# Optimization experiments

Hardware: AMD Instinct MI355X
Metric: run time of the kernel (lower is better)

The kernel has to match this reference:

```python
import jax, jax.numpy as jnp
import numpy as np

LORA_RANK = 16
LORA_ALPHA = 32.0
LORA_SCALE = LORA_ALPHA / LORA_RANK
W_BITS = 8
A_BITS = 8


def fake_quant(x, bits):
    """Symmetric per-tensor fake quantization with straight-through estimator."""
    qmax = 2.0 ** (bits - 1) - 1.0
    scale = jnp.maximum(jnp.max(jnp.abs(x)), 1e-8) / qmax
    q = jnp.clip(jnp.round(x / scale), -qmax, qmax) * scale
    return x + jax.lax.stop_gradient(q - x)  # STE


def quant_linear_lora(x, W, b, A, B):
    # x: [..., in], W: [out, in], A: [r, in], B: [out, r]
    xq = fake_quant(x, A_BITS)
    Wq = fake_quant(W, W_BITS)
    base = jnp.einsum('bsi,oi->bso', xq, Wq) + b
    lora = jnp.einsum('bsr,or->bso', jnp.einsum('bsi,ri->bsr', x, A), B)
    return base + LORA_SCALE * lora


def setup_inputs() -> dict:
    key = jax.random.key(0)
    ks = jax.random.split(key, 9)
    n_embd, d_ff, B_, S = 1024, 4096, 4, 2048
    s_in = 1.0 / np.sqrt(n_embd)
    s_ff = 1.0 / np.sqrt(d_ff)
    return {
        'hidden_states': jax.random.normal(ks[0], (B_, S, n_embd), jnp.float32),
        'W_fc': jax.random.normal(ks[1], (d_ff, n_embd), jnp.float32) * s_in,
        'b_fc': jax.random.normal(ks[2], (d_ff,), jnp.float32) * 0.02,
        'A_fc': jax.random.normal(ks[3], (LORA_RANK, n_embd), jnp.float32) * s_in,
        'B_fc': jax.random.normal(ks[4], (d_ff, LORA_RANK), jnp.float32) * 0.01,
        'W_proj': jax.random.normal(ks[5], (n_embd, d_ff), jnp.float32) * s_ff,
        'b_proj': jax.random.normal(ks[6], (n_embd,), jnp.float32) * 0.02,
        'A_proj': jax.random.normal(ks[7], (LORA_RANK, d_ff), jnp.float32) * s_ff,
        'B_proj': jax.random.normal(ks[8], (n_embd, LORA_RANK), jnp.float32) * 0.01,
    }


def reference(hidden_states, W_fc, b_fc, A_fc, B_fc, W_proj, b_proj, A_proj, B_proj):
    h = quant_linear_lora(hidden_states, W_fc, b_fc, A_fc, B_fc)
    h = jax.nn.gelu(h, approximate=False)  # nn.GELU() default = exact erf GELU
    h = quant_linear_lora(h, W_proj, b_proj, A_proj, B_proj)
    return h
```

## Files before the change

kernel.cpp:

```cpp
#include <hip/hip_runtime.h>
#include <stdint.h>

using i32x4 = __attribute__((ext_vector_type(4))) int;
using f32x4 = __attribute__((ext_vector_type(4))) float;
using f16x4 = __attribute__((ext_vector_type(4))) _Float16;

#define M_TOK 8192
#define N_EMB 1024
#define D_FF  4096

__device__ __forceinline__ void async_lds16(void* lds, const void* g) {
  __builtin_amdgcn_global_load_lds(
      (const __attribute__((address_space(1))) void*)g,
      (__attribute__((address_space(3))) void*)lds, 16, 0, 0);
}

__global__ void zero_slots_k(unsigned* s) {
  if (threadIdx.x < 16) s[threadIdx.x] = 0u;
}

__global__ void absmax_k(const float* __restrict__ p, long n, unsigned* __restrict__ slot) {
  long i = ((long)blockIdx.x * blockDim.x + threadIdx.x) * 4;
  long stride = (long)gridDim.x * blockDim.x * 4;
  float m = 0.f;
  for (; i < n; i += stride) {
    float4 v = *(const float4*)(p + i);
    m = fmaxf(m, fmaxf(fmaxf(fabsf(v.x), fabsf(v.y)), fmaxf(fabsf(v.z), fabsf(v.w))));
  }
  for (int o = 32; o; o >>= 1) m = fmaxf(m, __shfl_xor(m, o));
  __shared__ float sm[4];
  if ((threadIdx.x & 63) == 0) sm[threadIdx.x >> 6] = m;
  __syncthreads();
  if (threadIdx.x == 0) {
    m = fmaxf(fmaxf(sm[0], sm[1]), fmaxf(sm[2], sm[3]));
    atomicMax(slot, __float_as_uint(m));
  }
}

__global__ void quant_k(const float* __restrict__ p, int8_t* __restrict__ q, long n,
                        const unsigned* __restrict__ slot) {
  float inv = 127.f / fmaxf(__uint_as_float(*slot), 1e-8f);
  long i = ((long)blockIdx.x * blockDim.x + threadIdx.x) * 4;
  long stride = (long)gridDim.x * blockDim.x * 4;
  for (; i < n; i += stride) {
    float4 v = *(const float4*)(p + i);
    int b0 = (int)fminf(fmaxf(rintf(v.x * inv), -127.f), 127.f);
    int b1 = (int)fminf(fmaxf(rintf(v.y * inv), -127.f), 127.f);
    int b2 = (int)fminf(fmaxf(rintf(v.z * inv), -127.f), 127.f);
    int b3 = (int)fminf(fmaxf(rintf(v.w * inv), -127.f), 127.f);
    int w = (b0 & 0xff) | ((b1 & 0xff) << 8) | ((b2 & 0xff) << 16) | ((b3 & 0xff) << 24);
    *(int*)(q + i) = w;
  }
}

__global__ void prep_bfrag_k(const float* __restrict__ A, _Float16* __restrict__ Bp, int K) {
  int s = blockIdx.x;
  int l = threadIdx.x;
  int r = l & 15, g = l >> 4;
  float4 v = *(const float4*)(A + (long)r * K + s * 16 + g * 4);
  f16x4 h;
  h[0] = (_Float16)v.x; h[1] = (_Float16)v.y; h[2] = (_Float16)v.z; h[3] = (_Float16)v.w;
  *(f16x4*)(Bp + ((long)s * 64 + l) * 4) = h;
}

__global__ __launch_bounds__(512) void lora_quant_k(
    const float* __restrict__ X, const _Float16* __restrict__ Bpre,
    const unsigned* __restrict__ slot, int8_t* __restrict__ Q,
    float* __restrict__ T, int K) {
  int lane = threadIdx.x & 63, wave = threadIdx.x >> 6;
  int row0 = blockIdx.x * 16;
  int r = lane & 15, g = lane >> 4;
  float inv = 127.f / fmaxf(__uint_as_float(*slot), 1e-8f);

  int kPerWave = K >> 3;
  int kbase = wave * kPerWave;
  const float* xrow = X + (long)(row0 + r) * K;
  int8_t* qrow = Q + (long)(row0 + r) * K;

  f32x4 acc = {0.f, 0.f, 0.f, 0.f};
  int nsteps = kPerWave >> 4;
#pragma unroll 4
  for (int s = 0; s < nsteps; s++) {
    int k = kbase + s * 16 + g * 4;
    float4 v = *(const float4*)(xrow + k);
    int b0 = (int)fminf(fmaxf(rintf(v.x * inv), -127.f), 127.f);
    int b1 = (int)fminf(fmaxf(rintf(v.y * inv), -127.f), 127.f);
    int b2 = (int)fminf(fmaxf(rintf(v.z * inv), -127.f), 127.f);
    int b3 = (int)fminf(fmaxf(rintf(v.w * inv), -127.f), 127.f);
    *(int*)(qrow + k) = (b0 & 0xff) | ((b1 & 0xff) << 8) | ((b2 & 0xff) << 16) | ((b3 & 0xff) << 24);
    f16x4 a;
    a[0] = (_Float16)v.x; a[1] = (_Float16)v.y; a[2] = (_Float16)v.z; a[3] = (_Float16)v.w;
    int gs = (kbase + s * 16) >> 4;
    f16x4 b = *(const f16x4*)(Bpre + ((long)gs * 64 + lane) * 4);
    acc = __builtin_amdgcn_mfma_f32_16x16x16f16(a, b, acc, 0, 0, 0);
  }

  __shared__ float part[8][16][17];
#pragma unroll
  for (int j = 0; j < 4; j++) part[wave][g * 4 + j][r] = acc[j];
  __syncthreads();
  int t = threadIdx.x;
  if (t < 256) {
    int m = t >> 4, rr = t & 15;
    float sum = 0.f;
#pragma unroll
    for (int w = 0; w < 8; w++) sum += part[w][m][rr];
    T[(long)(row0 + m) * 16 + rr] = 2.0f * sum;
  }
}

template <bool GELU>
__global__ __launch_bounds__(256, 3) void gemm_q8(
    const int8_t* __restrict__ Aq, const int8_t* __restrict__ Bq,
    int M, int N, int K,
    const unsigned* __restrict__ sa, const unsigned* __restrict__ sb,
    const float* __restrict__ bias,
    const float* __restrict__ T,
    const float* __restrict__ Bl,
    float* __restrict__ C, unsigned* hmax) {
  __shared__ __align__(16) int8_t As[16384];
  __shared__ __align__(16) int8_t Bs[16384];

  int bn = blockIdx.x * 128;
  int bm = blockIdx.y * 128;

  int t = threadIdx.x;
  int lane = t & 63, wave = t >> 6;
  int wr = wave >> 1, wc = wave & 1;
  int l16 = lane & 15, lq = lane >> 4;

  int ldst[4];
  const int8_t* srcA[4];
  const int8_t* srcB[4];
#pragma unroll
  for (int i = 0; i < 4; i++) {
    int s = i * 256 + t;
    int row = s >> 3;
    int col = s & 7;
    ldst[i] = s * 16;
    srcA[i] = Aq + (long)(bm + row) * K + col * 16;
    srcB[i] = Bq + (long)(bn + row) * K + col * 16;
  }

  int aoff[4], boff[4];
#pragma unroll
  for (int mf = 0; mf < 4; mf++) aoff[mf] = (wr * 64 + mf * 16 + l16) * 128 + lq * 16;
#pragma unroll
  for (int nf = 0; nf < 4; nf++) boff[nf] = (wc * 64 + nf * 16 + l16) * 128 + lq * 16;

  i32x4 acc[4][4] = {};
  int KT = K >> 7;

  for (int kt = 0; kt < KT; ++kt) {
    long ko = (long)kt * 128;
#pragma unroll
    for (int i = 0; i < 4; i++) async_lds16(As + ldst[i], srcA[i] + ko);
#pragma unroll
    for (int i = 0; i < 4; i++) async_lds16(Bs + ldst[i], srcB[i] + ko);
    __syncthreads();

#pragma unroll
    for (int kh = 0; kh < 2; kh++) {
      int kx = kh * 64;
      i32x4 av[4], bv[4];
#pragma unroll
      for (int mf = 0; mf < 4; mf++) av[mf] = *(const i32x4*)(As + aoff[mf] + kx);
#pragma unroll
      for (int nf = 0; nf < 4; nf++) bv[nf] = *(const i32x4*)(Bs + boff[nf] + kx);
#pragma unroll
      for (int mf = 0; mf < 4; mf++)
#pragma unroll
        for (int nf = 0; nf < 4; nf++)
          acc[mf][nf] = __builtin_amdgcn_mfma_i32_16x16x64_i8(av[mf], bv[nf], acc[mf][nf], 0, 0, 0);
    }
    __syncthreads();
  }

  float s = (fmaxf(__uint_as_float(*sa), 1e-8f) * (1.f / 127.f)) *
            (fmaxf(__uint_as_float(*sb), 1e-8f) * (1.f / 127.f));

  f16x4 af[4], bf[4];
#pragma unroll
  for (int mf = 0; mf < 4; mf++) {
    int m = bm + wr * 64 + mf * 16 + l16;
    float4 tv = *(const float4*)(T + (long)m * 16 + lq * 4);
    f16x4 v; v[0] = (_Float16)tv.x; v[1] = (_Float16)tv.y; v[2] = (_Float16)tv.z; v[3] = (_Float16)tv.w;
    af[mf] = v;
  }
#pragma unroll
  for (int nf = 0; nf < 4; nf++) {
    int n = bn + wc * 64 + nf * 16 + l16;
    float4 bv4 = *(const float4*)(Bl + (long)n * 16 + lq * 4);
    f16x4 v; v[0] = (_Float16)bv4.x; v[1] = (_Float16)bv4.y; v[2] = (_Float16)bv4.z; v[3] = (_Float16)bv4.w;
    bf[nf] = v;
  }
  float bias_v[4];
#pragma unroll
  for (int nf = 0; nf < 4; nf++) bias_v[nf] = bias[bn + wc * 64 + nf * 16 + l16];

  float lmax = 0.f;
#pragma unroll
  for (int mf = 0; mf < 4; mf++) {
#pragma unroll
    for (int nf = 0; nf < 4; nf++) {
      f32x4 fa = __builtin_amdgcn_mfma_f32_16x16x16f16(af[mf], bf[nf], f32x4{0.f, 0.f, 0.f, 0.f}, 0, 0, 0);
      int n = bn + wc * 64 + nf * 16 + l16;
#pragma unroll
      for (int j = 0; j < 4; j++) {
        int m = bm + wr * 64 + mf * 16 + lq * 4 + j;
        float v = s * (float)acc[mf][nf][j] + bias_v[nf] + fa[j];
        if constexpr (GELU) {
          v = 0.5f * v * (1.0f + erff(v * 0.70710678118654752f));
          lmax = fmaxf(lmax, fabsf(v));
        }
        C[(long)m * N + n] = v;
      }
    }
  }
  if constexpr (GELU) {
    for (int o = 32; o; o >>= 1) lmax = fmaxf(lmax, __shfl_xor(lmax, o));
    if (lane == 0) atomicMax(hmax, __float_as_uint(lmax));
  }
}

extern "C" void kernel_launch(void* const* d_in, const int* in_sizes, int n_in,
                              void* d_out, int out_size, void* d_ws, size_t ws_size,
                              hipStream_t stream) {
  const float* x   = (const float*)d_in[0];
  const float* Wfc = (const float*)d_in[1];
  const float* bfc = (const float*)d_in[2];
  const float* Afc = (const float*)d_in[3];
  const float* Bfc = (const float*)d_in[4];
  const float* Wpj = (const float*)d_in[5];
  const float* bpj = (const float*)d_in[6];
  const float* Apj = (const float*)d_in[7];
  const float* Bpj = (const float*)d_in[8];
  float* out = (float*)d_out;

  char* ws = (char*)d_ws;
  unsigned* slots = (unsigned*)ws;
  int8_t* qx  = (int8_t*)(ws + 256);
  int8_t* qwf = qx  + (size_t)M_TOK * N_EMB;
  int8_t* qwp = qwf + (size_t)D_FF * N_EMB;
  int8_t* qh  = qwp + (size_t)N_EMB * D_FF;
  float*  t1  = (float*)(qh + (size_t)M_TOK * D_FF);
  float*  t2  = t1  + (size_t)M_TOK * 16;
  _Float16* Bp1 = (_Float16*)(t2 + (size_t)M_TOK * 16);
  _Float16* Bp2 = Bp1 + (size_t)N_EMB * 16;
  float*  h   = (float*)(Bp2 + (size_t)D_FF * 16);

  zero_slots_k<<<1, 64, 0, stream>>>(slots);
  absmax_k<<<1024, 256, 0, stream>>>(x,   (long)M_TOK * N_EMB, slots + 0);
  absmax_k<<<1024, 256, 0, stream>>>(Wfc, (long)D_FF * N_EMB,  slots + 1);
  absmax_k<<<1024, 256, 0, stream>>>(Wpj, (long)N_EMB * D_FF,  slots + 2);

  quant_k<<<2048, 256, 0, stream>>>(Wfc, qwf, (long)D_FF * N_EMB, slots + 1);
  quant_k<<<2048, 256, 0, stream>>>(Wpj, qwp, (long)N_EMB * D_FF, slots + 2);

  prep_bfrag_k<<<N_EMB / 16, 64, 0, stream>>>(Afc, Bp1, N_EMB);
  prep_bfrag_k<<<D_FF / 16, 64, 0, stream>>>(Apj, Bp2, D_FF);

  lora_quant_k<<<M_TOK / 16, 512, 0, stream>>>(x, Bp1, slots + 0, qx, t1, N_EMB);

  gemm_q8<true><<<dim3(D_FF / 128, M_TOK / 128), 256, 0, stream>>>(
      qx, qwf, M_TOK, D_FF, N_EMB, slots + 0, slots + 1, bfc, t1, Bfc, h, slots + 3);

  lora_quant_k<<<M_TOK / 16, 512, 0, stream>>>(h, Bp2, slots + 3, qh, t2, D_FF);

  gemm_q8<false><<<dim3(N_EMB / 128, M_TOK / 128), 256, 0, stream>>>(
      qh, qwp, M_TOK, N_EMB, D_FF, slots + 3, slots + 2, bpj, t2, Bpj, out, nullptr);
}
```

Before: 314.7 us.

## Store quantized operands as exact bf16 and use bf16 MFMA GEMMs

Quantized integer values are now stored as bf16 (exact for values up to 127) instead of int8, and both GEMMs switch from i8 MFMA 16x16x64 to bf16 MFMA 16x16x32 with a 64-wide K tile. This doubles the operand bytes and halves the math rate per instruction relative to int8, presumably to try a different MFMA path or to avoid some int8 issue. The launch-bounds occupancy hint is dropped and workspace buffers are reorganized, with qx aliasing qh.

```diff
diff --git a/kernel.cpp b/kernel.cpp
--- a/kernel.cpp
+++ b/kernel.cpp
@@ -1,9 +1,9 @@
 #include <hip/hip_runtime.h>
 #include <stdint.h>
 
-using i32x4 = __attribute__((ext_vector_type(4))) int;
-using f32x4 = __attribute__((ext_vector_type(4))) float;
-using f16x4 = __attribute__((ext_vector_type(4))) _Float16;
+using f32x4  = __attribute__((ext_vector_type(4))) float;
+using f16x4  = __attribute__((ext_vector_type(4))) _Float16;
+using bf16x8 = __attribute__((ext_vector_type(8))) short;
 
 #define M_TOK 8192
 #define N_EMB 1024
@@ -13,6 +13,10 @@
   __builtin_amdgcn_global_load_lds(
       (const __attribute__((address_space(1))) void*)g,
       (__attribute__((address_space(3))) void*)lds, 16, 0, 0);
+}
+
+__device__ __forceinline__ unsigned short bf16_exact(float f) {
+  return (unsigned short)(__float_as_uint(f) >> 16);
 }
 
 __global__ void zero_slots_k(unsigned* s) {
@@ -37,19 +41,19 @@
   }
 }
 
-__global__ void quant_k(const float* __restrict__ p, int8_t* __restrict__ q, long n,
+__global__ void quant_k(const float* __restrict__ p, unsigned short* __restrict__ q, long n,
                         const unsigned* __restrict__ slot) {
   float inv = 127.f / fmaxf(__uint_as_float(*slot), 1e-8f);
   long i = ((long)blockIdx.x * blockDim.x + threadIdx.x) * 4;
   long stride = (long)gridDim.x * blockDim.x * 4;
   for (; i < n; i += stride) {
     float4 v = *(const float4*)(p + i);
-    int b0 = (int)fminf(fmaxf(rintf(v.x * inv), -127.f), 127.f);
-    int b1 = (int)fminf(fmaxf(rintf(v.y * inv), -127.f), 127.f);
-    int b2 = (int)fminf(fmaxf(rintf(v.z * inv), -127.f), 127.f);
-    int b3 = (int)fminf(fmaxf(rintf(v.w * inv), -127.f), 127.f);
-    int w = (b0 & 0xff) | ((b1 & 0xff) << 8) | ((b2 & 0xff) << 16) | ((b3 & 0xff) << 24);
-    *(int*)(q + i) = w;
+    ushort4 w;
+    w.x = bf16_exact(fminf(fmaxf(rintf(v.x * inv), -127.f), 127.f));
+    w.y = bf16_exact(fminf(fmaxf(rintf(v.y * inv), -127.f), 127.f));
+    w.z = bf16_exact(fminf(fmaxf(rintf(v.z * inv), -127.f), 127.f));
+    w.w = bf16_exact(fminf(fmaxf(rintf(v.w * inv), -127.f), 127.f));
+    *(ushort4*)(q + i) = w;
   }
 }
 
@@ -65,7 +69,7 @@
 
 __global__ __launch_bounds__(512) void lora_quant_k(
     const float* __restrict__ X, const _Float16* __restrict__ Bpre,
-    const unsigned* __restrict__ slot, int8_t* __restrict__ Q,
+    const unsigned* __restrict__ slot, unsigned short* __restrict__ Q,
     float* __restrict__ T, int K) {
   int lane = threadIdx.x & 63, wave = threadIdx.x >> 6;
   int row0 = blockIdx.x * 16;
@@ -75,7 +79,7 @@
   int kPerWave = K >> 3;
   int kbase = wave * kPerWave;
   const float* xrow = X + (long)(row0 + r) * K;
-  int8_t* qrow = Q + (long)(row0 + r) * K;
+  unsigned short* qrow = Q + (long)(row0 + r) * K;
 
   f32x4 acc = {0.f, 0.f, 0.f, 0.f};
   int nsteps = kPerWave >> 4;
@@ -83,11 +87,12 @@
   for (int s = 0; s < nsteps; s++) {
     int k = kbase + s * 16 + g * 4;
     float4 v = *(const float4*)(xrow + k);
-    int b0 = (int)fminf(fmaxf(rintf(v.x * inv), -127.f), 127.f);
-    int b1 = (int)fminf(fmaxf(rintf(v.y * inv), -127.f), 127.f);
-    int b2 = (int)fminf(fmaxf(rintf(v.z * inv), -127.f), 127.f);
-    int b3 = (int)fminf(fmaxf(rintf(v.w * inv), -127.f), 127.f);
-    *(int*)(qrow + k) = (b0 & 0xff) | ((b1 & 0xff) << 8) | ((b2 & 0xff) << 16) | ((b3 & 0xff) << 24);
+    ushort4 w;
+    w.x = bf16_exact(fminf(fmaxf(rintf(v.x * inv), -127.f), 127.f));
+    w.y = bf16_exact(fminf(fmaxf(rintf(v.y * inv), -127.f), 127.f));
+    w.z = bf16_exact(fminf(fmaxf(rintf(v.z * inv), -127.f), 127.f));
+    w.w = bf16_exact(fminf(fmaxf(rintf(v.w * inv), -127.f), 127.f));
+    *(ushort4*)(qrow + k) = w;
     f16x4 a;
     a[0] = (_Float16)v.x; a[1] = (_Float16)v.y; a[2] = (_Float16)v.z; a[3] = (_Float16)v.w;
     int gs = (kbase + s * 16) >> 4;
@@ -110,16 +115,16 @@
 }
 
 template <bool GELU>
-__global__ __launch_bounds__(256, 3) void gemm_q8(
-    const int8_t* __restrict__ Aq, const int8_t* __restrict__ Bq,
-    int M, int N, int K,
+__global__ __launch_bounds__(256) void gemm_bf(
+    const unsigned short* __restrict__ Aq, const unsigned short* __restrict__ Bq,
+    int N, int K,
     const unsigned* __restrict__ sa, const unsigned* __restrict__ sb,
     const float* __restrict__ bias,
     const float* __restrict__ T,
     const float* __restrict__ Bl,
     float* __restrict__ C, unsigned* hmax) {
-  __shared__ __align__(16) int8_t As[16384];
-  __shared__ __align__(16) int8_t Bs[16384];
+  __shared__ __align__(16) unsigned short As[128 * 64];
+  __shared__ __align__(16) unsigned short Bs[128 * 64];
 
   int bn = blockIdx.x * 128;
   int bm = blockIdx.y * 128;
@@ -130,16 +135,16 @@
   int l16 = lane & 15, lq = lane >> 4;
 
   int ldst[4];
-  const int8_t* srcA[4];
-  const int8_t* srcB[4];
+  const unsigned short* srcA[4];
+  const unsigned short* srcB[4];
 #pragma unroll
   for (int i = 0; i < 4; i++) {
     int s = i * 256 + t;
     int row = s >> 3;
     int col = s & 7;
-    ldst[i] = s * 16;
-    srcA[i] = Aq + (long)(bm + row) * K + col * 16;
-    srcB[i] = Bq + (long)(bn + row) * K + col * 16;
+    ldst[i] = s * 8;
+    srcA[i] = Aq + (long)(bm + row) * K + col * 8;
+    srcB[i] = Bq + (long)(bn + row) * K + col * 8;
   }
 
   int aoff[4], boff[4];
@@ -148,11 +153,11 @@
 #pragma unroll
   for (int nf = 0; nf < 4; nf++) boff[nf] = (wc * 64 + nf * 16 + l16) * 128 + lq * 16;
 
-  i32x4 acc[4][4] = {};
-  int KT = K >> 7;
+  f32x4 acc[4][4] = {};
+  int KT = K >> 6;
 
   for (int kt = 0; kt < KT; ++kt) {
-    long ko = (long)kt * 128;
+    long ko = (long)kt * 64;
 #pragma unroll
     for (int i = 0; i < 4; i++) async_lds16(As + ldst[i], srcA[i] + ko);
 #pragma unroll
@@ -160,18 +165,20 @@
     __syncthreads();
 
 #pragma unroll
-    for (int kh = 0; kh < 2; kh++) {
-      int kx = kh * 64;
-      i32x4 av[4], bv[4];
-#pragma unroll
-      for (int mf = 0; mf < 4; mf++) av[mf] = *(const i32x4*)(As + aoff[mf] + kx);
-#pragma unroll
-      for (int nf = 0; nf < 4; nf++) bv[nf] = *(const i32x4*)(Bs + boff[nf] + kx);
+    for (int ks = 0; ks < 2; ks++) {
+      int kx = ks * 64;
+      bf16x8 av[4], bv[4];
 #pragma unroll
       for (int mf = 0; mf < 4; mf++)
+        av[mf] = *(const bf16x8*)((const char*)As + aoff[mf] + kx);
+#pragma unroll
+      for (int nf = 0; nf < 4; nf++)
+        bv[nf] = *(const bf16x8*)((const char*)Bs + boff[nf] + kx);
+#pragma unroll
+      for (int mf = 0; mf < 4; mf++)
 #pragma unroll
         for (int nf = 0; nf < 4; nf++)
-          acc[mf][nf] = __builtin_amdgcn_mfma_i32_16x16x64_i8(av[mf], bv[nf], acc[mf][nf], 0, 0, 0);
+          acc[mf][nf] = __builtin_amdgcn_mfma_f32_16x16x32_bf16(av[mf], bv[nf], acc[mf][nf], 0, 0, 0);
     }
     __syncthreads();
   }
@@ -208,7 +215,7 @@
 #pragma unroll
       for (int j = 0; j < 4; j++) {
         int m = bm + wr * 64 + mf * 16 + lq * 4 + j;
-        float v = s * (float)acc[mf][nf][j] + bias_v[nf] + fa[j];
+        float v = s * acc[mf][nf][j] + bias_v[nf] + fa[j];
         if constexpr (GELU) {
           v = 0.5f * v * (1.0f + erff(v * 0.70710678118654752f));
           lmax = fmaxf(lmax, fabsf(v));
@@ -239,15 +246,15 @@
 
   char* ws = (char*)d_ws;
   unsigned* slots = (unsigned*)ws;
-  int8_t* qx  = (int8_t*)(ws + 256);
-  int8_t* qwf = qx  + (size_t)M_TOK * N_EMB;
-  int8_t* qwp = qwf + (size_t)D_FF * N_EMB;
-  int8_t* qh  = qwp + (size_t)N_EMB * D_FF;
-  float*  t1  = (float*)(qh + (size_t)M_TOK * D_FF);
-  float*  t2  = t1  + (size_t)M_TOK * 16;
+  unsigned short* qwf = (unsigned short*)(ws + 256);
+  unsigned short* qwp = qwf + (size_t)D_FF * N_EMB;
+  float* t1 = (float*)(qwp + (size_t)N_EMB * D_FF);
+  float* t2 = t1 + (size_t)M_TOK * 16;
   _Float16* Bp1 = (_Float16*)(t2 + (size_t)M_TOK * 16);
   _Float16* Bp2 = Bp1 + (size_t)N_EMB * 16;
-  float*  h   = (float*)(Bp2 + (size_t)D_FF * 16);
+  float* h = (float*)(Bp2 + (size_t)D_FF * 16);
+  unsigned short* qh = (unsigned short*)(h + (size_t)M_TOK * D_FF);
+  unsigned short* qx = qh;
 
   zero_slots_k<<<1, 64, 0, stream>>>(slots);
   absmax_k<<<1024, 256, 0, stream>>>(x,   (long)M_TOK * N_EMB, slots + 0);
@@ -262,11 +269,11 @@
 
   lora_quant_k<<<M_TOK / 16, 512, 0, stream>>>(x, Bp1, slots + 0, qx, t1, N_EMB);
 
-  gemm_q8<true><<<dim3(D_FF / 128, M_TOK / 128), 256, 0, stream>>>(
-      qx, qwf, M_TOK, D_FF, N_EMB, slots + 0, slots + 1, bfc, t1, Bfc, h, slots + 3);
+  gemm_bf<true><<<dim3(D_FF / 128, M_TOK / 128), 256, 0, stream>>>(
+      qx, qwf, D_FF, N_EMB, slots + 0, slots + 1, bfc, t1, Bfc, h, slots + 3);
 
   lora_quant_k<<<M_TOK / 16, 512, 0, stream>>>(h, Bp2, slots + 3, qh, t2, D_FF);
 
-  gemm_q8<false><<<dim3(N_EMB / 128, M_TOK / 128), 256, 0, stream>>>(
-      qh, qwp, M_TOK, N_EMB, D_FF, slots + 3, slots + 2, bpj, t2, Bpj, out, nullptr);
-}
+  gemm_bf<false><<<dim3(N_EMB / 128, M_TOK / 128), 256, 0, stream>>>(
+      qh, qwp, N_EMB, D_FF, slots + 3, slots + 2, bpj, t2, Bpj, out, nullptr);
+}
```

New measurement: 411.2 us. +30.6%, slower.

## Switch int8 GEMM to 32x32x32 MFMA with XOR-swizzled LDS layout

Applied to the files above, without the earlier changes.

Replaces the 16x16x64 int8 MFMA tiles with 32x32x32 int8 MFMA (2x2 fragments per wave), which lowers LDS fragment reads per MFMA. It adds an XOR swizzle on the LDS column groups to avoid bank conflicts when loading the new fragments. The LoRA epilogue now uses the 32x32x16 f16 MFMA, and launch bounds go up to 4 blocks per CU. The risk is higher register pressure from 16-wide accumulators, and any error in the swizzle or output index mapping would break correctness.

```diff
diff --git a/kernel.cpp b/kernel.cpp
--- a/kernel.cpp
+++ b/kernel.cpp
@@ -1,9 +1,12 @@
 #include <hip/hip_runtime.h>
 #include <stdint.h>
 
-using i32x4 = __attribute__((ext_vector_type(4))) int;
-using f32x4 = __attribute__((ext_vector_type(4))) float;
-using f16x4 = __attribute__((ext_vector_type(4))) _Float16;
+using i32x4  = __attribute__((ext_vector_type(4))) int;
+using i32x16 = __attribute__((ext_vector_type(16))) int;
+using f32x4  = __attribute__((ext_vector_type(4))) float;
+using f32x16 = __attribute__((ext_vector_type(16))) float;
+using f16x4  = __attribute__((ext_vector_type(4))) _Float16;
+using f16x8  = __attribute__((ext_vector_type(8))) _Float16;
 
 #define M_TOK 8192
 #define N_EMB 1024
@@ -110,9 +113,9 @@
 }
 
 template <bool GELU>
-__global__ __launch_bounds__(256, 3) void gemm_q8(
+__global__ __launch_bounds__(256, 4) void gemm32(
     const int8_t* __restrict__ Aq, const int8_t* __restrict__ Bq,
-    int M, int N, int K,
+    int N, int K,
     const unsigned* __restrict__ sa, const unsigned* __restrict__ sb,
     const float* __restrict__ bias,
     const float* __restrict__ T,
@@ -127,7 +130,7 @@
   int t = threadIdx.x;
   int lane = t & 63, wave = t >> 6;
   int wr = wave >> 1, wc = wave & 1;
-  int l16 = lane & 15, lq = lane >> 4;
+  int l31 = lane & 31, l5 = lane >> 5;
 
   int ldst[4];
   const int8_t* srcA[4];
@@ -136,19 +139,25 @@
   for (int i = 0; i < 4; i++) {
     int s = i * 256 + t;
     int row = s >> 3;
-    int col = s & 7;
+    int cg = (s & 7) ^ (row & 7);
     ldst[i] = s * 16;
-    srcA[i] = Aq + (long)(bm + row) * K + col * 16;
-    srcB[i] = Bq + (long)(bn + row) * K + col * 16;
-  }
-
-  int aoff[4], boff[4];
-#pragma unroll
-  for (int mf = 0; mf < 4; mf++) aoff[mf] = (wr * 64 + mf * 16 + l16) * 128 + lq * 16;
-#pragma unroll
-  for (int nf = 0; nf < 4; nf++) boff[nf] = (wc * 64 + nf * 16 + l16) * 128 + lq * 16;
-
-  i32x4 acc[4][4] = {};
+    srcA[i] = Aq + (long)(bm + row) * K + cg * 16;
+    srcB[i] = Bq + (long)(bn + row) * K + cg * 16;
+  }
+
+  int aoff[2], boff[2];
+#pragma unroll
+  for (int mf = 0; mf < 2; mf++) {
+    int row = wr * 64 + mf * 32 + l31;
+    aoff[mf] = row * 128 + ((l5 ^ (row & 7)) << 4);
+  }
+#pragma unroll
+  for (int nf = 0; nf < 2; nf++) {
+    int row = wc * 64 + nf * 32 + l31;
+    boff[nf] = row * 128 + ((l5 ^ (row & 7)) << 4);
+  }
+
+  i32x16 acc[2][2] = {};
   int KT = K >> 7;
 
   for (int kt = 0; kt < KT; ++kt) {
@@ -160,18 +169,18 @@
     __syncthreads();
 
 #pragma unroll
-    for (int kh = 0; kh < 2; kh++) {
-      int kx = kh * 64;
-      i32x4 av[4], bv[4];
-#pragma unroll
-      for (int mf = 0; mf < 4; mf++) av[mf] = *(const i32x4*)(As + aoff[mf] + kx);
-#pragma unroll
-      for (int nf = 0; nf < 4; nf++) bv[nf] = *(const i32x4*)(Bs + boff[nf] + kx);
-#pragma unroll
-      for (int mf = 0; mf < 4; mf++)
-#pragma unroll
-        for (int nf = 0; nf < 4; nf++)
-          acc[mf][nf] = __builtin_amdgcn_mfma_i32_16x16x64_i8(av[mf], bv[nf], acc[mf][nf], 0, 0, 0);
+    for (int ks = 0; ks < 4; ks++) {
+      int kx = ks << 5;
+      i32x4 av[2], bv[2];
+#pragma unroll
+      for (int mf = 0; mf < 2; mf++) av[mf] = *(const i32x4*)(As + (aoff[mf] ^ kx));
+#pragma unroll
+      for (int nf = 0; nf < 2; nf++) bv[nf] = *(const i32x4*)(Bs + (boff[nf] ^ kx));
+#pragma unroll
+      for (int mf = 0; mf < 2; mf++)
+#pragma unroll
+        for (int nf = 0; nf < 2; nf++)
+          acc[mf][nf] = __builtin_amdgcn_mfma_i32_32x32x32_i8(av[mf], bv[nf], acc[mf][nf], 0, 0, 0);
     }
     __syncthreads();
   }
@@ -179,36 +188,30 @@
   float s = (fmaxf(__uint_as_float(*sa), 1e-8f) * (1.f / 127.f)) *
             (fmaxf(__uint_as_float(*sb), 1e-8f) * (1.f / 127.f));
 
-  f16x4 af[4], bf[4];
-#pragma unroll
-  for (int mf = 0; mf < 4; mf++) {
-    int m = bm + wr * 64 + mf * 16 + l16;
-    float4 tv = *(const float4*)(T + (long)m * 16 + lq * 4);
-    f16x4 v; v[0] = (_Float16)tv.x; v[1] = (_Float16)tv.y; v[2] = (_Float16)tv.z; v[3] = (_Float16)tv.w;
-    af[mf] = v;
-  }
-#pragma unroll
-  for (int nf = 0; nf < 4; nf++) {
-    int n = bn + wc * 64 + nf * 16 + l16;
-    float4 bv4 = *(const float4*)(Bl + (long)n * 16 + lq * 4);
-    f16x4 v; v[0] = (_Float16)bv4.x; v[1] = (_Float16)bv4.y; v[2] = (_Float16)bv4.z; v[3] = (_Float16)bv4.w;
-    bf[nf] = v;
-  }
-  float bias_v[4];
-#pragma unroll
-  for (int nf = 0; nf < 4; nf++) bias_v[nf] = bias[bn + wc * 64 + nf * 16 + l16];
-
   float lmax = 0.f;
 #pragma unroll
-  for (int mf = 0; mf < 4; mf++) {
-#pragma unroll
-    for (int nf = 0; nf < 4; nf++) {
-      f32x4 fa = __builtin_amdgcn_mfma_f32_16x16x16f16(af[mf], bf[nf], f32x4{0.f, 0.f, 0.f, 0.f}, 0, 0, 0);
-      int n = bn + wc * 64 + nf * 16 + l16;
-#pragma unroll
-      for (int j = 0; j < 4; j++) {
-        int m = bm + wr * 64 + mf * 16 + lq * 4 + j;
-        float v = s * (float)acc[mf][nf][j] + bias_v[nf] + fa[j];
+  for (int mf = 0; mf < 2; mf++) {
+    int m0 = bm + wr * 64 + mf * 32;
+    float4 t0 = *(const float4*)(T + (long)(m0 + l31) * 16 + l5 * 8);
+    float4 t1 = *(const float4*)(T + (long)(m0 + l31) * 16 + l5 * 8 + 4);
+    f16x8 tf;
+    tf[0] = (_Float16)t0.x; tf[1] = (_Float16)t0.y; tf[2] = (_Float16)t0.z; tf[3] = (_Float16)t0.w;
+    tf[4] = (_Float16)t1.x; tf[5] = (_Float16)t1.y; tf[6] = (_Float16)t1.z; tf[7] = (_Float16)t1.w;
+#pragma unroll
+    for (int nf = 0; nf < 2; nf++) {
+      int n = bn + wc * 64 + nf * 32 + l31;
+      float4 b0 = *(const float4*)(Bl + (long)n * 16 + l5 * 8);
+      float4 b1 = *(const float4*)(Bl + (long)n * 16 + l5 * 8 + 4);
+      f16x8 bf;
+      bf[0] = (_Float16)b0.x; bf[1] = (_Float16)b0.y; bf[2] = (_Float16)b0.z; bf[3] = (_Float16)b0.w;
+      bf[4] = (_Float16)b1.x; bf[5] = (_Float16)b1.y; bf[6] = (_Float16)b1.z; bf[7] = (_Float16)b1.w;
+      f32x16 fa = __builtin_amdgcn_mfma_f32_32x32x16_f16(tf, bf, (f32x16){}, 0, 0, 0);
+      float bias_v = bias[n];
+#pragma unroll
+      for (int reg = 0; reg < 16; reg++) {
+        int row = (reg & 3) + 8 * (reg >> 2) + 4 * l5;
+        int m = m0 + row;
+        float v = s * (float)acc[mf][nf][reg] + bias_v + fa[reg];
         if constexpr (GELU) {
           v = 0.5f * v * (1.0f + erff(v * 0.70710678118654752f));
           lmax = fmaxf(lmax, fabsf(v));
@@ -262,11 +265,11 @@
 
   lora_quant_k<<<M_TOK / 16, 512, 0, stream>>>(x, Bp1, slots + 0, qx, t1, N_EMB);
 
-  gemm_q8<true><<<dim3(D_FF / 128, M_TOK / 128), 256, 0, stream>>>(
-      qx, qwf, M_TOK, D_FF, N_EMB, slots + 0, slots + 1, bfc, t1, Bfc, h, slots + 3);
+  gemm32<true><<<dim3(D_FF / 128, M_TOK / 128), 256, 0, stream>>>(
+      qx, qwf, D_FF, N_EMB, slots + 0, slots + 1, bfc, t1, Bfc, h, slots + 3);
 
   lora_quant_k<<<M_TOK / 16, 512, 0, stream>>>(h, Bp2, slots + 3, qh, t2, D_FF);
 
-  gemm_q8<false><<<dim3(N_EMB / 128, M_TOK / 128), 256, 0, stream>>>(
-      qh, qwp, M_TOK, N_EMB, D_FF, slots + 3, slots + 2, bpj, t2, Bpj, out, nullptr);
-}
+  gemm32<false><<<dim3(N_EMB / 128, M_TOK / 128), 256, 0, stream>>>(
+      qh, qwp, N_EMB, D_FF, slots + 3, slots + 2, bpj, t2, Bpj, out, nullptr);
+}
```

After: 307.8 us. 2.2% less time.
